# Kernel optimization log

Hardware: AMD Instinct MI355X
Metric: run time of the kernel (lower is better)

The kernel has to match this reference:

```python
import jax, jax.numpy as jnp
import numpy as np

B, C, H, W = 64, 512, 32, 32
D = C // 8  # 64


def setup_inputs() -> dict:
    key = jax.random.key(0)
    k1, k2, k3, k4 = jax.random.split(key, 4)
    x = jax.random.normal(k1, (B, C, H, W), dtype=jnp.float32)
    query_m = jax.random.normal(k2, (H * W, D), dtype=jnp.float32)
    key_m = jax.random.normal(k3, (H * W, D), dtype=jnp.float32)
    # 1x1 conv C->C: weight [C_out, C_in], kaiming-ish scale
    value_w = jax.random.normal(k4, (C, C), dtype=jnp.float32) * (1.0 / np.sqrt(C))
    value_b = jnp.zeros((C,), dtype=jnp.float32)
    return {"x": x, "query_m": query_m, "key_m": key_m,
            "value_w": value_w, "value_b": value_b}


def reference(x, query_m, key_m, value_w, value_b):
    b, c, h, w = x.shape
    xf = x.reshape(b, c, h * w)                        # [B, C, N]
    q = jnp.einsum('bcn,nd->bcd', xf, query_m)         # [B, C, D]
    k = jnp.einsum('bcn,nd->bcd', xf, key_m)           # [B, C, D]
    energy = jnp.einsum('bcd,bed->bce', q, k)          # [B, C, C]
    energy = jax.nn.sigmoid(energy)
    attention = jax.nn.softmax(energy, axis=-2)        # softmax over rows (dim=-2)
    # 1x1 conv = channel matmul + bias
    v = jnp.einsum('bcn,oc->bon', xf, value_w) + value_b[None, :, None]  # [B, C, N]
    # out[b,j,n] = sum_i v[b,i,n] * attention[b,i,j]
    out = jnp.einsum('bin,bij->bjn', v, attention)     # [B, C, N]
    return out.reshape(b, c, h, w)
```

## Files before the change

### kernel.cpp

```cpp
#include <hip/hip_runtime.h>

#define BK 32

typedef __attribute__((ext_vector_type(8))) short bf16x8;
typedef __attribute__((ext_vector_type(4))) float f32x4;

__device__ __forceinline__ unsigned short f2bf(float f) {
  unsigned u = __builtin_bit_cast(unsigned, f);
  unsigned r = (u + 0x7FFFu + ((u >> 16) & 1u)) >> 16;
  return (unsigned short)r;
}
__device__ __forceinline__ float bf2f(unsigned short h) {
  return __builtin_bit_cast(float, (unsigned)h << 16);
}
__device__ __forceinline__ unsigned pack2(unsigned short a, unsigned short b) {
  return (unsigned)a | ((unsigned)b << 16);
}

__device__ __forceinline__ void gld_lds16(const void* g, void* l) {
  __builtin_amdgcn_global_load_lds(
      (const __attribute__((address_space(1))) unsigned int*)g,
      (__attribute__((address_space(3))) unsigned int*)l, 16, 0, 0);
}

#define SCHED0() __builtin_amdgcn_sched_barrier(0)
#define NTBAR() do { SCHED0(); __builtin_amdgcn_s_barrier(); SCHED0(); } while (0)
#define VMW(N) do { asm volatile("s_waitcnt vmcnt(" #N ")" ::: "memory"); SCHED0(); } while (0)
#define LGKM0() do { asm volatile("s_waitcnt lgkmcnt(0)" ::: "memory"); SCHED0(); } while (0)
#define MFMA16(a, b, c) __builtin_amdgcn_mfma_f32_16x16x32_bf16(a, b, c, 0, 0, 0)

__device__ __forceinline__ void split8_store(float4 v0, float4 v1,
                                             unsigned short* Hdst,
                                             unsigned short* Ldst) {
  float f[8] = {v0.x, v0.y, v0.z, v0.w, v1.x, v1.y, v1.z, v1.w};
  unsigned short hh[8], ll[8];
#pragma unroll
  for (int i = 0; i < 8; ++i) {
    hh[i] = f2bf(f[i]);
    ll[i] = f2bf(f[i] - bf2f(hh[i]));
  }
  *reinterpret_cast<uint4*>(Hdst) = make_uint4(pack2(hh[0], hh[1]), pack2(hh[2], hh[3]),
                                               pack2(hh[4], hh[5]), pack2(hh[6], hh[7]));
  *reinterpret_cast<uint4*>(Ldst) = make_uint4(pack2(ll[0], ll[1]), pack2(ll[2], ll[3]),
                                               pack2(ll[4], ll[5]), pack2(ll[6], ll[7]));
}

__global__ __launch_bounds__(256) void qkm_split(const float* __restrict__ Qm,
                                                 const float* __restrict__ Km,
                                                 unsigned short* __restrict__ Th,
                                                 unsigned short* __restrict__ Tl) {
  __shared__ float lt[64][65];
  int k0 = blockIdx.x * 64;
  int half = blockIdx.y;
  const float* M = half ? Km : Qm;
  int t = threadIdx.x;
  int cl = (t & 15) * 4;
  int rl = t >> 4;
#pragma unroll
  for (int rr = 0; rr < 4; ++rr) {
    int r = rl + rr * 16;
    float4 v = *reinterpret_cast<const float4*>(&M[(long)(k0 + r) * 64 + cl]);
    lt[cl + 0][r] = v.x;
    lt[cl + 1][r] = v.y;
    lt[cl + 2][r] = v.z;
    lt[cl + 3][r] = v.w;
  }
  __syncthreads();
#pragma unroll
  for (int rr = 0; rr < 4; ++rr) {
    int c = rl + rr * 16;
    unsigned short h[4], lo[4];
#pragma unroll
    for (int i = 0; i < 4; ++i) {
      float f = lt[c][cl + i];
      h[i] = f2bf(f);
      lo[i] = f2bf(f - bf2f(h[i]));
    }
    *reinterpret_cast<uint2*>(&Th[(long)(half * 64 + c) * 1024 + k0 + cl]) =
        make_uint2(pack2(h[0], h[1]), pack2(h[2], h[3]));
    *reinterpret_cast<uint2*>(&Tl[(long)(half * 64 + c) * 1024 + k0 + cl]) =
        make_uint2(pack2(lo[0], lo[1]), pack2(lo[2], lo[3]));
  }
}

__global__ __launch_bounds__(256) void k1_mfma(const float* __restrict__ x,
                                               const unsigned short* __restrict__ Th,
                                               const unsigned short* __restrict__ Tl,
                                               unsigned short* __restrict__ qkh,
                                               unsigned short* __restrict__ qkl,
                                               unsigned short* __restrict__ xbT) {
  __shared__ unsigned short Dh[2][128 * 32];
  __shared__ unsigned short Dl[2][128 * 32];
  __shared__ unsigned short Xh[2][64 * 32];
  __shared__ unsigned short Xl[2][64 * 32];
  const int t = threadIdx.x;
  const int l = t & 63;
  const int w = t >> 6;
  const int wr = w >> 1, wc = w & 1;
  const long mBase = (long)blockIdx.x * 64;
  const int b = blockIdx.x >> 3;
  const int cBase = (blockIdx.x & 7) * 64;

  f32x4 acc[4][2];
#pragma unroll
  for (int m = 0; m < 4; ++m)
#pragma unroll
    for (int n = 0; n < 2; ++n) acc[m][n] = (f32x4){0.f, 0.f, 0.f, 0.f};

  const int xrow_l = t >> 2;
  const int kslot = t & 3;
  const int xsl = kslot ^ ((t >> 3) & 3);
  const int srcslot = (l & 3) ^ ((l >> 3) & 3);
  const int frag_off = (l & 15) * 32 + ((((l >> 4) ^ (l >> 1)) & 3) * 8);
  const float* xrow = x + (mBase + xrow_l) * 1024;

#define K1_STAGE_B(k0, p)                                                     \
  {                                                                           \
    _Pragma("unroll") for (int c = 0; c < 2; ++c) {                           \
      int ch = c * 4 + w;                                                     \
      int row = ch * 16 + (l >> 2);                                           \
      gld_lds16(Th + (long)row * 1024 + (k0) + srcslot * 8, &Dh[p][ch * 512]);\
      gld_lds16(Tl + (long)row * 1024 + (k0) + srcslot * 8, &Dl[p][ch * 512]);\
    }                                                                         \
  }

#define K1_COMPUTE(p)                                                         \
  {                                                                           \
    bf16x8 dh[4], dl[4], xh[2], xl[2];                                        \
    _Pragma("unroll") for (int m = 0; m < 4; ++m) {                           \
      dh[m] = *reinterpret_cast<const bf16x8*>(&Dh[p][(wr * 64 + m * 16) * 32 + frag_off]); \
      dl[m] = *reinterpret_cast<const bf16x8*>(&Dl[p][(wr * 64 + m * 16) * 32 + frag_off]); \
    }                                                                         \
    _Pragma("unroll") for (int n = 0; n < 2; ++n) {                           \
      xh[n] = *reinterpret_cast<const bf16x8*>(&Xh[p][(wc * 32 + n * 16) * 32 + frag_off]); \
      xl[n] = *reinterpret_cast<const bf16x8*>(&Xl[p][(wc * 32 + n * 16) * 32 + frag_off]); \
    }                                                                         \
    _Pragma("unroll") for (int m = 0; m < 4; ++m)                             \
        _Pragma("unroll") for (int n = 0; n < 2; ++n) {                       \
      acc[m][n] = MFMA16(dh[m], xh[n], acc[m][n]);                            \
      acc[m][n] = MFMA16(dh[m], xl[n], acc[m][n]);                            \
      acc[m][n] = MFMA16(dl[m], xh[n], acc[m][n]);                            \
    }                                                                         \
  }

#define K1_WRITEBACK(p, kk)                                                   \
  {                                                                           \
    int n_loc = t >> 3;                                                       \
    int c0w = (t & 7) * 8;                                                    \
    unsigned short vv[8];                                                     \
    _Pragma("unroll") for (int i2 = 0; i2 < 8; ++i2) {                        \
      int r = c0w + i2;                                                       \
      int sl2 = (n_loc >> 3) ^ ((r >> 1) & 3);                                \
      vv[i2] = Xh[p][r * 32 + sl2 * 8 + (n_loc & 7)];                         \
    }                                                                         \
    *reinterpret_cast<uint4*>(                                                \
        &xbT[(long)b * 524288 + (long)((kk) + n_loc) * 512 + cBase + c0w]) =  \
        make_uint4(pack2(vv[0], vv[1]), pack2(vv[2], vv[3]),                  \
                   pack2(vv[4], vv[5]), pack2(vv[6], vv[7]));                 \
  }

  {
    float4 p0 = *reinterpret_cast<const float4*>(&xrow[kslot * 8]);
    float4 p1 = *reinterpret_cast<const float4*>(&xrow[kslot * 8 + 4]);
    K1_STAGE_B(0, 0);
    split8_store(p0, p1, &Xh[0][xrow_l * 32 + xsl * 8], &Xl[0][xrow_l * 32 + xsl * 8]);
  }

  for (int k0 = 0; k0 < 1024; k0 += 64) {
    __syncthreads();
    float4 na0 = *reinterpret_cast<const float4*>(&xrow[k0 + 32 + kslot * 8]);
    float4 na1 = *reinterpret_cast<const float4*>(&xrow[k0 + 32 + kslot * 8 + 4]);
    K1_STAGE_B(k0 + 32, 1);
    K1_COMPUTE(0);
    split8_store(na0, na1, &Xh[1][xrow_l * 32 + xsl * 8], &Xl[1][xrow_l * 32 + xsl * 8]);
    K1_WRITEBACK(0, k0);
    __syncthreads();
    if (k0 + 64 < 1024) {
      float4 nb0 = *reinterpret_cast<const float4*>(&xrow[k0 + 64 + kslot * 8]);
      float4 nb1 = *reinterpret_cast<const float4*>(&xrow[k0 + 64 + kslot * 8 + 4]);
      K1_STAGE_B(k0 + 64, 0);
      K1_COMPUTE(1);
      split8_store(nb0, nb1, &Xh[0][xrow_l * 32 + xsl * 8], &Xl[0][xrow_l * 32 + xsl * 8]);
      K1_WRITEBACK(1, k0 + 32);
    } else {
      K1_COMPUTE(1);
      K1_WRITEBACK(1, k0 + 32);
    }
  }

#pragma unroll
  for (int m = 0; m < 4; ++m)
#pragma unroll
    for (int n = 0; n < 2; ++n) {
      int d0 = wr * 64 + m * 16 + (l >> 4) * 4;
      long xr = mBase + wc * 32 + n * 16 + (l & 15);
      unsigned short h4[4], l4[4];
#pragma unroll
      for (int reg = 0; reg < 4; ++reg) {
        float v = acc[m][n][reg];
        h4[reg] = f2bf(v);
        l4[reg] = f2bf(v - bf2f(h4[reg]));
      }
      *reinterpret_cast<uint2*>(&qkh[xr * 128 + d0]) =
          make_uint2(pack2(h4[0], h4[1]), pack2(h4[2], h4[3]));
      *reinterpret_cast<uint2*>(&qkl[xr * 128 + d0]) =
          make_uint2(pack2(l4[0], l4[1]), pack2(l4[2], l4[3]));
    }
#undef K1_STAGE_B
#undef K1_COMPUTE
#undef K1_WRITEBACK
}

__global__ __launch_bounds__(256) void k2a_mfma(const unsigned short* __restrict__ qkh,
                                                const unsigned short* __restrict__ qkl,
                                                unsigned short* __restrict__ st) {
  __shared__ unsigned short Ah[128 * 64];
  __shared__ unsigned short Al[128 * 64];
  __shared__ unsigned short Bh[128 * 64];
  __shared__ unsigned short Bl[128 * 64];
  const int t = threadIdx.x;
  const int l = t & 63;
  const int w = t >> 6;
  const int wr = w >> 1, wc = w & 1;

  const int cpx = gridDim.x >> 3;
  const int orig = blockIdx.x;
  const int lw = (orig & 7) * cpx + (orig >> 3);
  const int b = lw >> 4;
  const int tile = lw & 15;
  const int iBase = (tile >> 2) * 128;
  const int jBase = (tile & 3) * 128;
  const long bq = (long)b * 512;

  const int sg = (l & 7) ^ (l >> 3);
#pragma unroll
  for (int c4 = 0; c4 < 4; ++c4) {
    int rb = w * 32 + c4 * 8;
    long rowA = bq + iBase + rb + (l >> 3);
    long rowB = bq + jBase + rb + (l >> 3);
    gld_lds16(qkh + rowA * 128 + sg * 8, &Ah[rb * 64]);
    gld_lds16(qkl + rowA * 128 + sg * 8, &Al[rb * 64]);
    gld_lds16(qkh + rowB * 128 + 64 + sg * 8, &Bh[rb * 64]);
    gld_lds16(qkl + rowB * 128 + 64 + sg * 8, &Bl[rb * 64]);
  }
  __syncthreads();

  f32x4 acc[4][4];
#pragma unroll
  for (int m = 0; m < 4; ++m)
#pragma unroll
    for (int n = 0; n < 4; ++n) acc[m][n] = (f32x4){0.f, 0.f, 0.f, 0.f};

#pragma unroll
  for (int ks = 0; ks < 2; ++ks) {
    bf16x8 ah[4], al4[4], bh[4], bl4[4];
#pragma unroll
    for (int m = 0; m < 4; ++m) {
      int row = wr * 64 + m * 16 + (l & 15);
      int off = row * 64 + ((ks * 4 + (l >> 4)) ^ (row & 7)) * 8;
      ah[m] = *reinterpret_cast<const bf16x8*>(&Ah[off]);
      al4[m] = *reinterpret_cast<const bf16x8*>(&Al[off]);
    }
#pragma unroll
    for (int n = 0; n < 4; ++n) {
      int row = wc * 64 + n * 16 + (l & 15);
      int off = row * 64 + ((ks * 4 + (l >> 4)) ^ (row & 7)) * 8;
      bh[n] = *reinterpret_cast<const bf16x8*>(&Bh[off]);
      bl4[n] = *reinterpret_cast<const bf16x8*>(&Bl[off]);
    }
#pragma unroll
    for (int m = 0; m < 4; ++m)
#pragma unroll
      for (int n = 0; n < 4; ++n) {
        acc[m][n] = MFMA16(ah[m], bh[n], acc[m][n]);
        acc[m][n] = MFMA16(ah[m], bl4[n], acc[m][n]);
        acc[m][n] = MFMA16(al4[m], bh[n], acc[m][n]);
      }
  }

  unsigned short* sb = st + (long)b * 512 * 512;
#pragma unroll
  for (int m = 0; m < 4; ++m)
#pragma unroll
    for (int n = 0; n < 4; ++n) {
      int i0 = iBase + wr * 64 + m * 16 + (l >> 4) * 4;
      int j = jBase + wc * 64 + n * 16 + (l & 15);
      unsigned short p[4];
#pragma unroll
      for (int reg = 0; reg < 4; ++reg) {
        float sg2 = 1.0f / (1.0f + __expf(-acc[m][n][reg]));
        p[reg] = f2bf(__expf(sg2));
      }
      *reinterpret_cast<uint2*>(&sb[(long)j * 512 + i0]) = *reinterpret_cast<uint2*>(p);
    }
}

__global__ __launch_bounds__(256) void k2b_rsum(const unsigned short* __restrict__ st,
                                                const float* __restrict__ bias,
                                                float* __restrict__ rsum,
                                                float* __restrict__ attbias) {
  int jg = blockIdx.x * 4 + (threadIdx.x >> 6);
  int l = threadIdx.x & 63;
  const unsigned short* row = st + (long)jg * 512 + l * 8;
  ushort4 u0 = *reinterpret_cast<const ushort4*>(row);
  ushort4 u1 = *reinterpret_cast<const ushort4*>(row + 4);
  float4 b0 = *reinterpret_cast<const float4*>(&bias[l * 8]);
  float4 b1 = *reinterpret_cast<const float4*>(&bias[l * 8 + 4]);
  float f0 = bf2f(u0.x), f1 = bf2f(u0.y), f2 = bf2f(u0.z), f3 = bf2f(u0.w);
  float f4 = bf2f(u1.x), f5 = bf2f(u1.y), f6 = bf2f(u1.z), f7 = bf2f(u1.w);
  float sum = (f0 + f1) + (f2 + f3) + ((f4 + f5) + (f6 + f7));
  float sumb = f0 * b0.x + f1 * b0.y + f2 * b0.z + f3 * b0.w +
               f4 * b1.x + f5 * b1.y + f6 * b1.z + f7 * b1.w;
#pragma unroll
  for (int off = 32; off > 0; off >>= 1) {
    sum += __shfl_down(sum, off);
    sumb += __shfl_down(sumb, off);
  }
  if (l == 0) {
    float r = 1.0f / sum;
    rsum[jg] = r;
    attbias[jg] = sumb * r;
  }
}

__global__ __launch_bounds__(256) void transpose_conv(const float* __restrict__ in,
                                                      unsigned short* __restrict__ out,
                                                      int inRows, int inCols,
                                                      long inBatch, long outBatch) {
  __shared__ unsigned short lt[64][65];
  int b = blockIdx.z;
  int r0 = blockIdx.y * 64;
  int c0 = blockIdx.x * 64;
  const float* I = in + (long)b * inBatch;
  unsigned short* O = out + (long)b * outBatch;
  int t = threadIdx.x;
  int cl = (t & 15) * 4;
  int rl = t >> 4;
#pragma unroll
  for (int rr = 0; rr < 4; ++rr) {
    int r = rl + rr * 16;
    float4 v = *reinterpret_cast<const float4*>(&I[(long)(r0 + r) * inCols + c0 + cl]);
    lt[cl + 0][r] = f2bf(v.x);
    lt[cl + 1][r] = f2bf(v.y);
    lt[cl + 2][r] = f2bf(v.z);
    lt[cl + 3][r] = f2bf(v.w);
  }
  __syncthreads();
#pragma unroll
  for (int rr = 0; rr < 4; ++rr) {
    int c = rl + rr * 16;
    unsigned short v[4] = {lt[c][cl], lt[c][cl + 1], lt[c][cl + 2], lt[c][cl + 3]};
    *reinterpret_cast<uint2*>(&O[(long)(c0 + c) * inRows + r0 + cl]) =
        *reinterpret_cast<uint2*>(&v[0]);
  }
}

template <int MODE>
__global__ __launch_bounds__(512) void mfma_nt256(const unsigned short* __restrict__ Abase,
                                                  const unsigned short* __restrict__ Bbase,
                                                  const float* __restrict__ rowscale,
                                                  unsigned short* __restrict__ Wout,
                                                  float* __restrict__ Fout) {
  __shared__ unsigned short As[2][256 * 64];
  __shared__ unsigned short Bs[2][256 * 64];
  const int t = threadIdx.x;
  const int l = t & 63;
  const int w = t >> 6;
  const int wr = w >> 2;
  const int wc = w & 3;

  const int cpx = gridDim.x >> 3;
  const int orig = blockIdx.x;
  const int lw = (orig & 7) * cpx + (orig >> 3);
  const int TPB_SH = (MODE == 0) ? 2 : 3;
  const int b = lw >> TPB_SH;
  const int tile = lw & ((1 << TPB_SH) - 1);
  const int mBase = (tile >> 1) * 256;
  const int nBase = (tile & 1) * 256;

  const unsigned short* Ag = Abase + ((MODE == 0) ? 0L : (long)b * (1024 * 512)) + (long)mBase * 512;
  const unsigned short* Bg = Bbase + (long)b * (512 * 512) + (long)nBase * 512;

  f32x4 acc[8][4];
#pragma unroll
  for (int m = 0; m < 8; ++m)
#pragma unroll
    for (int n = 0; n < 4; ++n) acc[m][n] = (f32x4){0.f, 0.f, 0.f, 0.f};

  const int srcslot = (l & 7) ^ (l >> 3);
  const int so0 = ((l >> 4) ^ (l & 7)) * 8;
  const int so1 = ((4 + (l >> 4)) ^ (l & 7)) * 8;

#define STG_A(p, tt, pr)                                                       \
  gld_lds16(Ag + (long)((pr) * 64 + w * 8 + (l >> 3)) * 512 + (tt) * 64 + srcslot * 8, \
            &As[p][((pr) * 64 + w * 8) * 64]);
#define STG_B(p, tt, pr)                                                       \
  gld_lds16(Bg + (long)((pr) * 64 + w * 8 + (l >> 3)) * 512 + (tt) * 64 + srcslot * 8, \
            &Bs[p][((pr) * 64 + w * 8) * 64]);

#define PHASE(p, q, STAGE_STMT, VMSTMT)                                        \
  {                                                                            \
    bf16x8 a00 = *reinterpret_cast<const bf16x8*>(                             \
        &As[p][(wr * 128 + (2 * (q)) * 16 + (l & 15)) * 64 + so0]);            \
    bf16x8 a01 = *reinterpret_cast<const bf16x8*>(                             \
        &As[p][(wr * 128 + (2 * (q)) * 16 + (l & 15)) * 64 + so1]);            \
    bf16x8 a10 = *reinterpret_cast<const bf16x8*>(                             \
        &As[p][(wr * 128 + (2 * (q) + 1) * 16 + (l & 15)) * 64 + so0]);        \
    bf16x8 a11 = *reinterpret_cast<const bf16x8*>(                             \
        &As[p][(wr * 128 + (2 * (q) + 1) * 16 + (l & 15)) * 64 + so1]);        \
    if ((q) == 0) {                                                            \
      _Pragma("unroll") for (int n = 0; n < 4; ++n) {                          \
        bfr0[n] = *reinterpret_cast<const bf16x8*>(                            \
            &Bs[p][(wc * 64 + n * 16 + (l & 15)) * 64 + so0]);                 \
        bfr1[n] = *reinterpret_cast<const bf16x8*>(                            \
            &Bs[p][(wc * 64 + n * 16 + (l & 15)) * 64 + so1]);                 \
      }                                                                        \
    }                                                                          \
    STAGE_STMT;                                                                \
    SCHED0();                                                                  \
    __builtin_amdgcn_s_barrier();                                              \
    LGKM0();                                                                   \
    __builtin_amdgcn_s_setprio(1);                                             \
    _Pragma("unroll") for (int n = 0; n < 4; ++n) {                            \
      acc[2 * (q)][n] = MFMA16(a00, bfr0[n], acc[2 * (q)][n]);                 \
      acc[2 * (q)][n] = MFMA16(a01, bfr1[n], acc[2 * (q)][n]);                 \
      acc[2 * (q) + 1][n] = MFMA16(a10, bfr0[n], acc[2 * (q) + 1][n]);         \
      acc[2 * (q) + 1][n] = MFMA16(a11, bfr1[n], acc[2 * (q) + 1][n]);         \
    }                                                                          \
    __builtin_amdgcn_s_setprio(0);                                             \
    VMSTMT;                                                                    \
    NTBAR();                                                                   \
  }

  bf16x8 bfr0[4], bfr1[4];

  STG_A(0, 0, 0); STG_A(0, 0, 1); STG_A(0, 0, 2); STG_A(0, 0, 3);
  STG_B(0, 0, 0); STG_B(0, 0, 1); STG_B(0, 0, 2); STG_B(0, 0, 3);
  STG_B(1, 1, 0); STG_B(1, 1, 1); STG_B(1, 1, 2); STG_B(1, 1, 3);
  STG_A(1, 1, 0); STG_A(1, 1, 2);
  VMW(6);
  NTBAR();

  for (int it = 0; it < 4; ++it) {
    const int t1 = 2 * it + 1;
    const int t2 = (2 * it + 2 < 8) ? 2 * it + 2 : 7;
    const int t3 = (2 * it + 3 < 8) ? 2 * it + 3 : 7;
    PHASE(0, 0, { STG_A(1, t1, 1); STG_A(1, t1, 3); }, );
    PHASE(0, 1, { STG_B(0, t2, 0); STG_B(0, t2, 1); }, VMW(10));
    PHASE(0, 2, { STG_B(0, t2, 2); STG_B(0, t2, 3); }, );
    PHASE(0, 3, { STG_A(0, t2, 0); STG_A(0, t2, 2); }, VMW(8));
    PHASE(1, 0, { STG_A(0, t2, 1); STG_A(0, t2, 3); }, );
    PHASE(1, 1, { STG_B(1, t3, 0); STG_B(1, t3, 1); }, VMW(10));
    PHASE(1, 2, { STG_B(1, t3, 2); STG_B(1, t3, 3); }, );
    PHASE(1, 3, { STG_A(1, t3, 0); STG_A(1, t3, 2); }, VMW(8));
  }
#undef PHASE
#undef STG_A
#undef STG_B

  if (MODE == 0) {
    unsigned short* W = Wout + (long)b * (512 * 512);
#pragma unroll
    for (int n = 0; n < 4; ++n) {
      int j = nBase + wc * 64 + n * 16 + (l & 15);
      float rs = rowscale[b * 512 + j];
#pragma unroll
      for (int m = 0; m < 8; ++m) {
        int c0 = mBase + wr * 128 + m * 16 + (l >> 4) * 4;
        unsigned short p[4];
#pragma unroll
        for (int reg = 0; reg < 4; ++reg) p[reg] = f2bf(acc[m][n][reg] * rs);
        *reinterpret_cast<uint2*>(&W[(long)j * 512 + c0]) = *reinterpret_cast<uint2*>(p);
      }
    }
  } else {
    float* O = Fout + (long)b * (512 * 1024);
#pragma unroll
    for (int n = 0; n < 4; ++n) {
      int j = nBase + wc * 64 + n * 16 + (l & 15);
      float ab = rowscale[b * 512 + j];
#pragma unroll
      for (int m = 0; m < 8; ++m) {
        int n0 = mBase + wr * 128 + m * 16 + (l >> 4) * 4;
        *reinterpret_cast<float4*>(&O[(long)j * 1024 + n0]) =
            make_float4(acc[m][n][0] + ab, acc[m][n][1] + ab,
                        acc[m][n][2] + ab, acc[m][n][3] + ab);
      }
    }
  }
}

extern "C" void kernel_launch(void* const* d_in, const int* in_sizes, int n_in,
                              void* d_out, int out_size, void* d_ws, size_t ws_size,
                              hipStream_t stream) {
  const float* x  = (const float*)d_in[0];
  const float* Qm = (const float*)d_in[1];
  const float* Km = (const float*)d_in[2];
  const float* vw = (const float*)d_in[3];
  const float* vb = (const float*)d_in[4];
  float* out = (float*)d_out;

  float* ws = (float*)d_ws;
  unsigned short* qkh  = (unsigned short*)ws;
  unsigned short* qkl  = qkh + 4194304;
  unsigned short* st   = (unsigned short*)(ws + 4194304);
  unsigned short* weff = (unsigned short*)(ws + 4194304 + 8388608);
  unsigned short* xbT  = (unsigned short*)(ws + 4194304 + 16777216);
  unsigned short* vwT  = (unsigned short*)(ws + 4194304 + 33554432);
  unsigned short* qkTh = (unsigned short*)(ws + 4194304 + 33554432 + 131072);
  unsigned short* qkTl = qkTh + 131072;
  float* rsum    = ws + 4194304 + 33554432 + 131072 + 131072;
  float* attbias = rsum + 32768;

  transpose_conv<<<dim3(8, 8, 1), 256, 0, stream>>>(vw, vwT, 512, 512, 0L, 0L);
  qkm_split<<<dim3(16, 2), 256, 0, stream>>>(Qm, Km, qkTh, qkTl);
  k1_mfma<<<512, 256, 0, stream>>>(x, qkTh, qkTl, qkh, qkl, xbT);
  k2a_mfma<<<1024, 256, 0, stream>>>(qkh, qkl, st);
  k2b_rsum<<<8192, 256, 0, stream>>>(st, vb, rsum, attbias);
  mfma_nt256<0><<<256, 512, 0, stream>>>(vwT, st, rsum, weff, nullptr);
  mfma_nt256<1><<<512, 512, 0, stream>>>(xbT, weff, attbias, nullptr, out);
}
```

Measured before the change: 204.8 us.

## Restructure k1 to per-wave 32-row tiles with direct register fragment loads

Rewrites the first projection kernel so each wave owns 32 rows of x and all 128 output columns, loading x and the split Q/K matrices straight from global memory into MFMA fragments instead of staging them through shared LDS with block barriers. The x tile is double-buffered in registers. A small per-wave LDS buffer now does only the transpose for the bf16 xbT output. The grid is halved to 256 blocks. This removes __syncthreads and the LDS staging, but every wave re-reads the full Th/Tl matrices from global or cache, and per-wave register use grows with 16 accumulators.

```diff
diff --git a/kernel.cpp b/kernel.cpp
--- a/kernel.cpp
+++ b/kernel.cpp
@@ -1,6 +1,4 @@
 #include <hip/hip_runtime.h>
-
-#define BK 32
 
 typedef __attribute__((ext_vector_type(8))) short bf16x8;
 typedef __attribute__((ext_vector_type(4))) float f32x4;
@@ -29,20 +27,22 @@
 #define LGKM0() do { asm volatile("s_waitcnt lgkmcnt(0)" ::: "memory"); SCHED0(); } while (0)
 #define MFMA16(a, b, c) __builtin_amdgcn_mfma_f32_16x16x32_bf16(a, b, c, 0, 0, 0)
 
-__device__ __forceinline__ void split8_store(float4 v0, float4 v1,
-                                             unsigned short* Hdst,
-                                             unsigned short* Ldst) {
+__device__ __forceinline__ void split8_frag(float4 v0, float4 v1,
+                                            bf16x8* H, bf16x8* L,
+                                            unsigned short hh[8]) {
   float f[8] = {v0.x, v0.y, v0.z, v0.w, v1.x, v1.y, v1.z, v1.w};
-  unsigned short hh[8], ll[8];
+  unsigned short ll[8];
 #pragma unroll
   for (int i = 0; i < 8; ++i) {
     hh[i] = f2bf(f[i]);
     ll[i] = f2bf(f[i] - bf2f(hh[i]));
   }
-  *reinterpret_cast<uint4*>(Hdst) = make_uint4(pack2(hh[0], hh[1]), pack2(hh[2], hh[3]),
-                                               pack2(hh[4], hh[5]), pack2(hh[6], hh[7]));
-  *reinterpret_cast<uint4*>(Ldst) = make_uint4(pack2(ll[0], ll[1]), pack2(ll[2], ll[3]),
-                                               pack2(ll[4], ll[5]), pack2(ll[6], ll[7]));
+  uint4 hv = make_uint4(pack2(hh[0], hh[1]), pack2(hh[2], hh[3]),
+                        pack2(hh[4], hh[5]), pack2(hh[6], hh[7]));
+  uint4 lv = make_uint4(pack2(ll[0], ll[1]), pack2(ll[2], ll[3]),
+                        pack2(ll[4], ll[5]), pack2(ll[6], ll[7]));
+  *H = __builtin_bit_cast(bf16x8, hv);
+  *L = __builtin_bit_cast(bf16x8, lv);
 }
 
 __global__ __launch_bounds__(256) void qkm_split(const float* __restrict__ Qm,
@@ -89,111 +89,94 @@
                                                unsigned short* __restrict__ qkh,
                                                unsigned short* __restrict__ qkl,
                                                unsigned short* __restrict__ xbT) {
-  __shared__ unsigned short Dh[2][128 * 32];
-  __shared__ unsigned short Dl[2][128 * 32];
-  __shared__ unsigned short Xh[2][64 * 32];
-  __shared__ unsigned short Xl[2][64 * 32];
+  __shared__ unsigned short Tt[4][32 * 40];
   const int t = threadIdx.x;
   const int l = t & 63;
   const int w = t >> 6;
-  const int wr = w >> 1, wc = w & 1;
-  const long mBase = (long)blockIdx.x * 64;
-  const int b = blockIdx.x >> 3;
-  const int cBase = (blockIdx.x & 7) * 64;
-
-  f32x4 acc[4][2];
-#pragma unroll
-  for (int m = 0; m < 4; ++m)
+  const long rowbase = ((long)blockIdx.x * 4 + w) * 32;
+  const int b = (int)(rowbase >> 9);
+  const int cB = (int)(rowbase & 511);
+  unsigned short* Ttw = Tt[w];
+
+  const int fr = l & 15;
+  const int fk = l >> 4;
+
+  const float* xr0 = x + (rowbase + fr) * 1024 + fk * 8;
+  const float* xr1 = x + (rowbase + 16 + fr) * 1024 + fk * 8;
+  const unsigned short* ThF = Th + (long)fr * 1024 + fk * 8;
+  const unsigned short* TlF = Tl + (long)fr * 1024 + fk * 8;
+
+  f32x4 acc[8][2];
+#pragma unroll
+  for (int m = 0; m < 8; ++m)
 #pragma unroll
     for (int n = 0; n < 2; ++n) acc[m][n] = (f32x4){0.f, 0.f, 0.f, 0.f};
 
-  const int xrow_l = t >> 2;
-  const int kslot = t & 3;
-  const int xsl = kslot ^ ((t >> 3) & 3);
-  const int srcslot = (l & 3) ^ ((l >> 3) & 3);
-  const int frag_off = (l & 15) * 32 + ((((l >> 4) ^ (l >> 1)) & 3) * 8);
-  const float* xrow = x + (mBase + xrow_l) * 1024;
-
-#define K1_STAGE_B(k0, p)                                                     \
-  {                                                                           \
-    _Pragma("unroll") for (int c = 0; c < 2; ++c) {                           \
-      int ch = c * 4 + w;                                                     \
-      int row = ch * 16 + (l >> 2);                                           \
-      gld_lds16(Th + (long)row * 1024 + (k0) + srcslot * 8, &Dh[p][ch * 512]);\
-      gld_lds16(Tl + (long)row * 1024 + (k0) + srcslot * 8, &Dl[p][ch * 512]);\
-    }                                                                         \
-  }
-
-#define K1_COMPUTE(p)                                                         \
-  {                                                                           \
-    bf16x8 dh[4], dl[4], xh[2], xl[2];                                        \
-    _Pragma("unroll") for (int m = 0; m < 4; ++m) {                           \
-      dh[m] = *reinterpret_cast<const bf16x8*>(&Dh[p][(wr * 64 + m * 16) * 32 + frag_off]); \
-      dl[m] = *reinterpret_cast<const bf16x8*>(&Dl[p][(wr * 64 + m * 16) * 32 + frag_off]); \
-    }                                                                         \
-    _Pragma("unroll") for (int n = 0; n < 2; ++n) {                           \
-      xh[n] = *reinterpret_cast<const bf16x8*>(&Xh[p][(wc * 32 + n * 16) * 32 + frag_off]); \
-      xl[n] = *reinterpret_cast<const bf16x8*>(&Xl[p][(wc * 32 + n * 16) * 32 + frag_off]); \
-    }                                                                         \
-    _Pragma("unroll") for (int m = 0; m < 4; ++m)                             \
-        _Pragma("unroll") for (int n = 0; n < 2; ++n) {                       \
-      acc[m][n] = MFMA16(dh[m], xh[n], acc[m][n]);                            \
-      acc[m][n] = MFMA16(dh[m], xl[n], acc[m][n]);                            \
-      acc[m][n] = MFMA16(dl[m], xh[n], acc[m][n]);                            \
-    }                                                                         \
-  }
-
-#define K1_WRITEBACK(p, kk)                                                   \
-  {                                                                           \
-    int n_loc = t >> 3;                                                       \
-    int c0w = (t & 7) * 8;                                                    \
-    unsigned short vv[8];                                                     \
-    _Pragma("unroll") for (int i2 = 0; i2 < 8; ++i2) {                        \
-      int r = c0w + i2;                                                       \
-      int sl2 = (n_loc >> 3) ^ ((r >> 1) & 3);                                \
-      vv[i2] = Xh[p][r * 32 + sl2 * 8 + (n_loc & 7)];                         \
-    }                                                                         \
-    *reinterpret_cast<uint4*>(                                                \
-        &xbT[(long)b * 524288 + (long)((kk) + n_loc) * 512 + cBase + c0w]) =  \
-        make_uint4(pack2(vv[0], vv[1]), pack2(vv[2], vv[3]),                  \
-                   pack2(vv[4], vv[5]), pack2(vv[6], vv[7]));                 \
-  }
-
-  {
-    float4 p0 = *reinterpret_cast<const float4*>(&xrow[kslot * 8]);
-    float4 p1 = *reinterpret_cast<const float4*>(&xrow[kslot * 8 + 4]);
-    K1_STAGE_B(0, 0);
-    split8_store(p0, p1, &Xh[0][xrow_l * 32 + xsl * 8], &Xl[0][xrow_l * 32 + xsl * 8]);
-  }
-
-  for (int k0 = 0; k0 < 1024; k0 += 64) {
-    __syncthreads();
-    float4 na0 = *reinterpret_cast<const float4*>(&xrow[k0 + 32 + kslot * 8]);
-    float4 na1 = *reinterpret_cast<const float4*>(&xrow[k0 + 32 + kslot * 8 + 4]);
-    K1_STAGE_B(k0 + 32, 1);
-    K1_COMPUTE(0);
-    split8_store(na0, na1, &Xh[1][xrow_l * 32 + xsl * 8], &Xl[1][xrow_l * 32 + xsl * 8]);
-    K1_WRITEBACK(0, k0);
-    __syncthreads();
-    if (k0 + 64 < 1024) {
-      float4 nb0 = *reinterpret_cast<const float4*>(&xrow[k0 + 64 + kslot * 8]);
-      float4 nb1 = *reinterpret_cast<const float4*>(&xrow[k0 + 64 + kslot * 8 + 4]);
-      K1_STAGE_B(k0 + 64, 0);
-      K1_COMPUTE(1);
-      split8_store(nb0, nb1, &Xh[0][xrow_l * 32 + xsl * 8], &Xl[0][xrow_l * 32 + xsl * 8]);
-      K1_WRITEBACK(1, k0 + 32);
-    } else {
-      K1_COMPUTE(1);
-      K1_WRITEBACK(1, k0 + 32);
-    }
-  }
-
-#pragma unroll
-  for (int m = 0; m < 4; ++m)
+  float4 xa0, xa1, xa2, xa3, xb0, xb1, xb2, xb3;
+  xa0 = *reinterpret_cast<const float4*>(xr0);
+  xa1 = *reinterpret_cast<const float4*>(xr0 + 4);
+  xa2 = *reinterpret_cast<const float4*>(xr1);
+  xa3 = *reinterpret_cast<const float4*>(xr1 + 4);
+
+#define K1_BODY(ktc, XC0, XC1, XC2, XC3, XN0, XN1, XN2, XN3)                   \
+  {                                                                            \
+    const int ktn = ((ktc) + 1 < 32) ? (ktc) + 1 : 31;                         \
+    uint4 ah[8], al[8];                                                        \
+    _Pragma("unroll") for (int m = 0; m < 8; ++m) {                            \
+      ah[m] = *reinterpret_cast<const uint4*>(ThF + (long)m * 16384 + (ktc) * 32); \
+      al[m] = *reinterpret_cast<const uint4*>(TlF + (long)m * 16384 + (ktc) * 32); \
+    }                                                                          \
+    XN0 = *reinterpret_cast<const float4*>(xr0 + ktn * 32);                    \
+    XN1 = *reinterpret_cast<const float4*>(xr0 + ktn * 32 + 4);                \
+    XN2 = *reinterpret_cast<const float4*>(xr1 + ktn * 32);                    \
+    XN3 = *reinterpret_cast<const float4*>(xr1 + ktn * 32 + 4);                \
+    bf16x8 bh0, bl0, bh1, bl1;                                                 \
+    unsigned short hh0[8], hh1[8];                                             \
+    split8_frag(XC0, XC1, &bh0, &bl0, hh0);                                    \
+    split8_frag(XC2, XC3, &bh1, &bl1, hh1);                                    \
+    _Pragma("unroll") for (int i = 0; i < 8; ++i) {                            \
+      int k = fk * 8 + i;                                                      \
+      int s = (k >> 2) & 3;                                                    \
+      Ttw[k * 40 + ((((fr >> 3)) ^ s) << 3) + (fr & 7)] = hh0[i];              \
+      Ttw[k * 40 + (((2 + (fr >> 3)) ^ s) << 3) + (fr & 7)] = hh1[i];          \
+    }                                                                          \
+    _Pragma("unroll") for (int m = 0; m < 8; ++m) {                            \
+      bf16x8 Ah = __builtin_bit_cast(bf16x8, ah[m]);                           \
+      bf16x8 Al = __builtin_bit_cast(bf16x8, al[m]);                           \
+      acc[m][0] = MFMA16(Ah, bh0, acc[m][0]);                                  \
+      acc[m][0] = MFMA16(Ah, bl0, acc[m][0]);                                  \
+      acc[m][0] = MFMA16(Al, bh0, acc[m][0]);                                  \
+      acc[m][1] = MFMA16(Ah, bh1, acc[m][1]);                                  \
+      acc[m][1] = MFMA16(Ah, bl1, acc[m][1]);                                  \
+      acc[m][1] = MFMA16(Al, bh1, acc[m][1]);                                  \
+    }                                                                          \
+    LGKM0();                                                                   \
+    {                                                                          \
+      int k0 = l >> 2, ch = l & 3;                                             \
+      int s0 = (k0 >> 2) & 3;                                                  \
+      int k1i = k0 + 16;                                                       \
+      int s1 = (k1i >> 2) & 3;                                                 \
+      uint4 v0 = *reinterpret_cast<const uint4*>(&Ttw[k0 * 40 + ((ch ^ s0) << 3)]); \
+      uint4 v1 = *reinterpret_cast<const uint4*>(&Ttw[k1i * 40 + ((ch ^ s1) << 3)]); \
+      LGKM0();                                                                 \
+      long basex = (long)b * 524288 + cB + ch * 8;                             \
+      *reinterpret_cast<uint4*>(&xbT[basex + (long)((ktc) * 32 + k0) * 512]) = v0;  \
+      *reinterpret_cast<uint4*>(&xbT[basex + (long)((ktc) * 32 + k1i) * 512]) = v1; \
+    }                                                                          \
+  }
+
+  for (int kt = 0; kt < 32; kt += 2) {
+    K1_BODY(kt, xa0, xa1, xa2, xa3, xb0, xb1, xb2, xb3);
+    K1_BODY(kt + 1, xb0, xb1, xb2, xb3, xa0, xa1, xa2, xa3);
+  }
+#undef K1_BODY
+
+#pragma unroll
+  for (int m = 0; m < 8; ++m)
 #pragma unroll
     for (int n = 0; n < 2; ++n) {
-      int d0 = wr * 64 + m * 16 + (l >> 4) * 4;
-      long xr = mBase + wc * 32 + n * 16 + (l & 15);
+      int d0 = m * 16 + (l >> 4) * 4;
+      long xr = rowbase + n * 16 + (l & 15);
       unsigned short h4[4], l4[4];
 #pragma unroll
       for (int reg = 0; reg < 4; ++reg) {
@@ -206,9 +189,6 @@
       *reinterpret_cast<uint2*>(&qkl[xr * 128 + d0]) =
           make_uint2(pack2(l4[0], l4[1]), pack2(l4[2], l4[3]));
     }
-#undef K1_STAGE_B
-#undef K1_COMPUTE
-#undef K1_WRITEBACK
 }
 
 __global__ __launch_bounds__(256) void k2a_mfma(const unsigned short* __restrict__ qkh,
@@ -514,7 +494,7 @@
 
   transpose_conv<<<dim3(8, 8, 1), 256, 0, stream>>>(vw, vwT, 512, 512, 0L, 0L);
   qkm_split<<<dim3(16, 2), 256, 0, stream>>>(Qm, Km, qkTh, qkTl);
-  k1_mfma<<<512, 256, 0, stream>>>(x, qkTh, qkTl, qkh, qkl, xbT);
+  k1_mfma<<<256, 256, 0, stream>>>(x, qkTh, qkTl, qkh, qkl, xbT);
   k2a_mfma<<<1024, 256, 0, stream>>>(qkh, qkl, st);
   k2b_rsum<<<8192, 256, 0, stream>>>(st, vb, rsum, attbias);
   mfma_nt256<0><<<256, 512, 0, stream>>>(vwT, st, rsum, weff, nullptr);
```

After: 243.9 us. 19.1% more time.
